# Kernel optimization log

Hardware: AMD Instinct MI355X
Metric: run time of the kernel (lower is better)

The kernel has to match this reference:

```python
import jax, jax.numpy as jnp
import numpy as np

BRANCH = 16   # children per internal node
DEPTH = 4     # levels 0..4, leaves at level 4
IN = 512
HID = 512

def _level_sizes():
    return [BRANCH ** d for d in range(DEPTH + 1)]

def setup_inputs() -> dict:
    key = jax.random.key(0)
    ks = jax.random.split(key, 9)
    N = sum(_level_sizes())  # 69905
    x = jax.random.normal(ks[0], (N, IN), dtype=jnp.float32)
    s = 1.0 / np.sqrt(IN + HID)  # torch nn.Linear default init bound
    def lin(kw, kb):
        w = jax.random.uniform(kw, (HID, IN + HID), jnp.float32, -s, s)
        b = jax.random.uniform(kb, (HID,), jnp.float32, -s, s)
        return w, b
    wi_w, wi_b = lin(ks[1], ks[2])
    wf_w, wf_b = lin(ks[3], ks[4])
    wo_w, wo_b = lin(ks[5], ks[6])
    wu_w, wu_b = lin(ks[7], ks[8])
    return {"x": x, "wi_w": wi_w, "wi_b": wi_b, "wf_w": wf_w, "wf_b": wf_b,
            "wo_w": wo_w, "wo_b": wo_b, "wu_w": wu_w, "wu_b": wu_b}

def reference(x, wi_w, wi_b, wf_w, wf_b, wo_w, wo_b, wu_w, wu_b):
    sizes = _level_sizes()
    offs = np.concatenate([[0], np.cumsum(sizes)])
    levels = [x[offs[d]:offs[d + 1]] for d in range(DEPTH + 1)]

    def gates(xh):
        i = jax.nn.sigmoid(xh @ wi_w.T + wi_b)
        o = jax.nn.sigmoid(xh @ wo_w.T + wo_b)
        u = jnp.tanh(xh @ wu_w.T + wu_b)
        return i, o, u

    # leaf_forward: h_prev = 0, no forget terms
    Xl = levels[DEPTH]
    xh = jnp.concatenate([Xl, jnp.zeros((Xl.shape[0], HID), Xl.dtype)], axis=1)
    i, o, u = gates(xh)
    C = i * u
    H = o * jnp.tanh(C)

    # node_forward, bottom-up. Faithful quirk of the source: the forget gate
    # is computed on the child CELL state (cat(x, c_k)), not the hidden state.
    for d in range(DEPTH - 1, -1, -1):
        Xd = levels[d]                      # [n, IN]
        n = Xd.shape[0]
        Hc = H.reshape(n, BRANCH, HID)      # children hidden
        Cc = C.reshape(n, BRANCH, HID)      # children cell
        h_sum = Hc.sum(axis=1)
        xh = jnp.concatenate([Xd, h_sum], axis=1)
        i, o, u = gates(xh)
        xc = jnp.concatenate([jnp.broadcast_to(Xd[:, None, :], (n, BRANCH, IN)), Cc], axis=-1)
        f = jax.nn.sigmoid(jnp.einsum('nbk,hk->nbh', xc, wf_w) + wf_b)
        C = i * u + (f * Cc).sum(axis=1)
        H = o * jnp.tanh(C)

    return H[0], C[0]
```

## Files before the change

### kernel.cpp

```cpp
#include <hip/hip_runtime.h>
#include <stdint.h>
#include <stddef.h>


typedef __bf16 bf16x8 __attribute__((ext_vector_type(8)));
typedef float  f32x4  __attribute__((ext_vector_type(4)));
typedef void __attribute__((address_space(3))) lds_void_t;
typedef void __attribute__((address_space(1))) gbl_void_t;

__device__ __forceinline__ uint16_t f2bf(float f) {
  union { __bf16 b; uint16_t u; } v;
  v.b = (__bf16)f;
  return v.u;
}
__device__ __forceinline__ float bf2f(uint16_t u) {
  union { uint32_t u; float f; } v; v.u = (uint32_t)u << 16;
  return v.f;
}
__device__ __forceinline__ float sig_(float x) {
  return __builtin_amdgcn_rcpf(1.0f + __expf(-x));
}
__device__ __forceinline__ float tanh_(float x) {
  return __builtin_fmaf(2.f,
      __builtin_amdgcn_rcpf(1.f + __expf(-2.f * x)), -1.f);
}

__global__ void k_conv_all(const float4* __restrict__ x,
                           ushort4* __restrict__ xdst, long n4x,
                           const float4* __restrict__ w0,
                           const float4* __restrict__ w1,
                           const float4* __restrict__ w2,
                           const float4* __restrict__ w3,
                           ushort4* __restrict__ wdst) {
  const long per4 = (long)512 * 1024 / 4;
  const long total = n4x + 4 * per4;
  long i = blockIdx.x * (long)blockDim.x + threadIdx.x;
  long stride = (long)gridDim.x * blockDim.x;
  for (; i < total; i += stride) {
    float4 v;
    ushort4* d;
    if (i < n4x) {
      v = x[i];
      d = xdst + i;
    } else {
      long j = i - n4x;
      long seg = j / per4, off2 = j - seg * per4;
      const float4* s = (seg == 0) ? w0 : (seg == 1) ? w1
                       : (seg == 2) ? w2 : w3;
      v = s[off2];
      d = wdst + j;
    }
    ushort4 r;
    r.x = f2bf(v.x); r.y = f2bf(v.y); r.z = f2bf(v.z); r.w = f2bf(v.w);
    *d = r;
  }
}

#define BM 128
#define BN 128
#define BK 32

__global__ __launch_bounds__(256, 3)
void k_leaf_fx(const uint16_t* __restrict__ Xleaf,
               const uint16_t* __restrict__ Wg,
               const float* __restrict__ bi, const float* __restrict__ bo,
               const float* __restrict__ bu,
               uint16_t* __restrict__ Cbf,
               const uint16_t* __restrict__ Xnext,
               uint16_t* __restrict__ xh_next,
               const uint16_t* __restrict__ Xbf,
               const uint16_t* __restrict__ Wf,
               float* __restrict__ FxAll) {
  __shared__ uint16_t smem[20480];
  const int tid = threadIdx.x, lane = tid & 63, wave = tid >> 6;
  const int lrow = lane & 15, quad = lane >> 4;

  if (blockIdx.x < 4096) {
    uint16_t* As = smem;
    uint16_t* Bs = smem + 8192;
    const int wm = (wave >> 1) * 64, wn = (wave & 1) * 32;
    long tm, tn;
    {
      const int nTm = 512;
      int b = blockIdx.x;
      int x = b & 7, j = b >> 3, per = nTm >> 3;
      tn = j & 7; tm = (long)x * per + (j >> 3);
    }
    f32x4 acc[3][4][2] = {};
    const int srow = lane >> 3;
    const int scol = (((lane & 7) ^ srow) << 3);
    const int rsw = lrow & 7;
    const int pc[2] = { ((0 + quad) ^ rsw) << 3, ((4 + quad) ^ rsw) << 3 };

    for (int k0 = 0; k0 < 512; k0 += 64) {
#pragma unroll
      for (int j = 0; j < 4; ++j) {
        int grp = wave * 4 + j;
        int row = grp * 8 + srow;
        const uint16_t* gp = Xleaf + (tm * 128 + row) * 512L + k0 + scol;
        __builtin_amdgcn_global_load_lds((gbl_void_t*)(uintptr_t)gp,
            (lds_void_t*)&As[grp * 512], 16, 0, 0);
      }
#pragma unroll
      for (int j = 0; j < 6; ++j) {
        int cc = wave * 6 + j;
        int g  = cc >> 3;
        long grow = (long)g * 512 + tn * 64 + (cc & 7) * 8 + srow;
        const uint16_t* gp = Wg + grow * 1024 + k0 + scol;
        __builtin_amdgcn_global_load_lds((gbl_void_t*)(uintptr_t)gp,
            (lds_void_t*)&Bs[cc * 512], 16, 0, 0);
      }
      __syncthreads();
#pragma unroll
      for (int h = 0; h < 2; ++h) {
        bf16x8 a[4];
#pragma unroll
        for (int f = 0; f < 4; ++f)
          a[f] = *(const bf16x8*)&As[(wm + f * 16 + lrow) * 64 + pc[h]];
#pragma unroll
        for (int g = 0; g < 3; ++g) {
          bf16x8 b0 = *(const bf16x8*)&Bs[(g * 64 + wn + lrow) * 64 + pc[h]];
          bf16x8 b1 = *(const bf16x8*)&Bs[(g * 64 + wn + 16 + lrow) * 64 +
                                          pc[h]];
#pragma unroll
          for (int fm = 0; fm < 4; ++fm) {
            acc[g][fm][0] = __builtin_amdgcn_mfma_f32_16x16x32_bf16(
                a[fm], b0, acc[g][fm][0], 0, 0, 0);
            acc[g][fm][1] = __builtin_amdgcn_mfma_f32_16x16x32_bf16(
                a[fm], b1, acc[g][fm][1], 0, 0, 0);
          }
        }
      }
      __syncthreads();
    }
#pragma unroll
    for (int fn = 0; fn < 2; ++fn) {
      long col = tn * 64 + wn + fn * 16 + lrow;
      float biv = bi[col], bov = bo[col], buv = bu[col];
#pragma unroll
      for (int fm = 0; fm < 4; ++fm) {
        long row0 = tm * 128 + wm + fm * 16 + quad * 4;
        long pg   = tm * 8 + (wm >> 4) + fm;
        float hs = 0.f;
#pragma unroll
        for (int r = 0; r < 4; ++r) {
          long row = row0 + r;
          float iv = sig_(acc[0][fm][fn][r] + biv);
          float ov = sig_(acc[1][fm][fn][r] + bov);
          float uv = tanh_(acc[2][fm][fn][r] + buv);
          float c  = iv * uv;
          Cbf[row * 512 + col] = f2bf(c);
          hs += ov * tanh_(c);
        }
        hs += __shfl_xor(hs, 16, 64);
        hs += __shfl_xor(hs, 32, 64);
        if (quad == 0) {
          xh_next[pg * 1024 + col]       = Xnext[pg * 512 + col];
          xh_next[pg * 1024 + 512 + col] = f2bf(hs);
        }
      }
    }
  } else {
    uint16_t* As = smem;
    uint16_t* Bs = smem + 4096;
    const int wm = (wave >> 1) * 64, wn = (wave & 1) * 64;
    int bid2 = (int)blockIdx.x - 4096;
    const long tm = bid2 % 35, tn = bid2 / 35;
    f32x4 acc[4][4] = {};
    const int srow2 = lane >> 2, scol2 = (lane & 3) * 8;
    for (int k0 = 0; k0 < 512; k0 += BK) {
#pragma unroll
      for (int i = 0; i < 2; ++i) {
        int row = i * 64 + wave * 16 + srow2;
        const uint16_t* gp = Xbf + (tm * BM + row) * 512L + k0 + scol2;
        __builtin_amdgcn_global_load_lds((gbl_void_t*)(uintptr_t)gp,
            (lds_void_t*)&As[i * 2048 + wave * 512], 16, 0, 0);
      }
#pragma unroll
      for (int i = 0; i < 2; ++i) {
        int row = i * 64 + wave * 16 + srow2;
        const uint16_t* gp = Wf + (tn * BN + row) * 1024L + k0 + scol2;
        __builtin_amdgcn_global_load_lds((gbl_void_t*)(uintptr_t)gp,
            (lds_void_t*)&Bs[i * 2048 + wave * 512], 16, 0, 0);
      }
      __syncthreads();
      bf16x8 a[4], b[4];
#pragma unroll
      for (int f = 0; f < 4; ++f)
        a[f] = *(const bf16x8*)&As[(wm + f * 16 + lrow) * BK + quad * 8];
#pragma unroll
      for (int f = 0; f < 4; ++f)
        b[f] = *(const bf16x8*)&Bs[(wn + f * 16 + lrow) * BK + quad * 8];
#pragma unroll
      for (int fm = 0; fm < 4; ++fm)
#pragma unroll
        for (int fn = 0; fn < 4; ++fn)
          acc[fm][fn] = __builtin_amdgcn_mfma_f32_16x16x32_bf16(
              a[fm], b[fn], acc[fm][fn], 0, 0, 0);
      __syncthreads();
    }
#pragma unroll
    for (int fm = 0; fm < 4; ++fm)
#pragma unroll
      for (int fn = 0; fn < 4; ++fn) {
        long col  = tn * BN + wn + fn * 16 + lrow;
        long row0 = tm * BM + wm + fm * 16 + quad * 4;
#pragma unroll
        for (int r = 0; r < 4; ++r)
          FxAll[(row0 + r) * 512 + col] = acc[fm][fn][r];
      }
  }
}

template <bool HAS_F, int MF>
__global__ __launch_bounds__(256, 3)
void k_level(const uint16_t* __restrict__ A, int lda, int K,
             const uint16_t* __restrict__ Wg,
             const float* __restrict__ bi, const float* __restrict__ bo,
             const float* __restrict__ bu,
             const float* __restrict__ Fpart,
             uint16_t* __restrict__ Cbf,
             const uint16_t* __restrict__ Xnext,
             uint16_t* __restrict__ xh_next) {
  constexpr int BMT = MF * 32;
  __shared__ uint16_t As[BMT * 64];
  __shared__ uint16_t Bs[192 * 64];
  const int tid = threadIdx.x, lane = tid & 63, wave = tid >> 6;
  const int lrow = lane & 15, quad = lane >> 4;
  const int wm = (wave >> 1) * (MF * 16), wn = (wave & 1) * 32;

  long tm, tn;
  {
    const int nTm = (int)(gridDim.x >> 3);
    int b = blockIdx.x;
    if ((nTm & 7) == 0) {
      int x = b & 7, j = b >> 3, per = nTm >> 3;
      tn = j & 7; tm = (long)x * per + (j >> 3);
    } else { tm = b >> 3; tn = b & 7; }
  }

  f32x4 acc[3][MF][2] = {};

  const int srow = lane >> 3;
  const int scol = (((lane & 7) ^ srow) << 3);
  const int rsw = lrow & 7;
  const int pc[2] = { ((0 + quad) ^ rsw) << 3, ((4 + quad) ^ rsw) << 3 };

  for (int k0 = 0; k0 < K; k0 += 64) {
#pragma unroll
    for (int j = 0; j < MF; ++j) {
      int grp = wave * MF + j;
      int row = grp * 8 + srow;
      const uint16_t* gp = A + (tm * BMT + row) * (long)lda + k0 + scol;
      __builtin_amdgcn_global_load_lds((gbl_void_t*)(uintptr_t)gp,
          (lds_void_t*)&As[grp * 512], 16, 0, 0);
    }
#pragma unroll
    for (int j = 0; j < 6; ++j) {
      int cc = wave * 6 + j;
      int g  = cc >> 3;
      long grow = (long)g * 512 + tn * 64 + (cc & 7) * 8 + srow;
      const uint16_t* gp = Wg + grow * 1024 + k0 + scol;
      __builtin_amdgcn_global_load_lds((gbl_void_t*)(uintptr_t)gp,
          (lds_void_t*)&Bs[cc * 512], 16, 0, 0);
    }
    __syncthreads();

#pragma unroll
    for (int h = 0; h < 2; ++h) {
      bf16x8 a[MF];
#pragma unroll
      for (int f = 0; f < MF; ++f)
        a[f] = *(const bf16x8*)&As[(wm + f * 16 + lrow) * 64 + pc[h]];
#pragma unroll
      for (int g = 0; g < 3; ++g) {
        bf16x8 b0 = *(const bf16x8*)&Bs[(g * 64 + wn + lrow) * 64 + pc[h]];
        bf16x8 b1 = *(const bf16x8*)&Bs[(g * 64 + wn + 16 + lrow) * 64 +
                                        pc[h]];
#pragma unroll
        for (int fm = 0; fm < MF; ++fm) {
          acc[g][fm][0] = __builtin_amdgcn_mfma_f32_16x16x32_bf16(
              a[fm], b0, acc[g][fm][0], 0, 0, 0);
          acc[g][fm][1] = __builtin_amdgcn_mfma_f32_16x16x32_bf16(
              a[fm], b1, acc[g][fm][1], 0, 0, 0);
        }
      }
    }
    __syncthreads();
  }

#pragma unroll
  for (int fn = 0; fn < 2; ++fn) {
    long col = tn * 64 + wn + fn * 16 + lrow;
    float biv = bi[col], bov = bo[col], buv = bu[col];
#pragma unroll
    for (int fm = 0; fm < MF; ++fm) {
      long row0 = tm * BMT + wm + fm * 16 + quad * 4;
      long pg   = tm * (BMT / 16) + (wm >> 4) + fm;
      float hs = 0.f;
#pragma unroll
      for (int r = 0; r < 4; ++r) {
        long row = row0 + r;
        float iv = sig_(acc[0][fm][fn][r] + biv);
        float ov = sig_(acc[1][fm][fn][r] + bov);
        float uv = tanh_(acc[2][fm][fn][r] + buv);
        float c  = iv * uv;
        if (HAS_F) c += Fpart[row * 512 + col];
        Cbf[row * 512 + col] = f2bf(c);
        hs += ov * tanh_(c);
      }
      hs += __shfl_xor(hs, 16, 64);
      hs += __shfl_xor(hs, 32, 64);
      if (quad == 0) {
        xh_next[pg * 1024 + col]       = Xnext[pg * 512 + col];
        xh_next[pg * 1024 + 512 + col] = f2bf(hs);
      }
    }
  }
}

template <int MF>
__global__ __launch_bounds__(256, 3)
void k_fc_combine(const uint16_t* __restrict__ Cbf,
                  const uint16_t* __restrict__ Wfc, int ldb,
                  const float* __restrict__ Fx,
                  const float* __restrict__ bfb,
                  float* __restrict__ Fpart) {
  constexpr int BMT = MF * 32;
  __shared__ uint16_t As[BMT * 64];
  __shared__ uint16_t Bs[128 * 64];
  const int tid = threadIdx.x, lane = tid & 63, wave = tid >> 6;
  const int lrow = lane & 15, quad = lane >> 4;
  const int wm = (wave >> 1) * (MF * 16), wn = (wave & 1) * 64;
  long tm, tn;
  {
    const int nTm = (int)(gridDim.x >> 2);
    int b = blockIdx.x;
    if ((nTm & 7) == 0) {
      int x = b & 7, j = b >> 3, per = nTm >> 3;
      tn = j & 3; tm = (long)x * per + (j >> 2);
    } else { tm = b >> 2; tn = b & 3; }
  }
  const int lda = 512;
  f32x4 acc[MF][4] = {};

  const int srow = lane >> 3;
  const int scol = (((lane & 7) ^ srow) << 3);
  const int rsw = lrow & 7;
  const int pc[2] = { ((0 + quad) ^ rsw) << 3, ((4 + quad) ^ rsw) << 3 };

  for (int k0 = 0; k0 < 512; k0 += 64) {
#pragma unroll
    for (int j = 0; j < MF; ++j) {
      int grp = wave * MF + j;
      int row = grp * 8 + srow;
      const uint16_t* gp = Cbf + (tm * BMT + row) * (long)lda + k0 + scol;
      __builtin_amdgcn_global_load_lds((gbl_void_t*)(uintptr_t)gp,
          (lds_void_t*)&As[grp * 512], 16, 0, 0);
    }
#pragma unroll
    for (int j = 0; j < 4; ++j) {
      int row = wave * 32 + j * 8 + srow;
      const uint16_t* gp = Wfc + (tn * BN + row) * (long)ldb + k0 + scol;
      __builtin_amdgcn_global_load_lds((gbl_void_t*)(uintptr_t)gp,
          (lds_void_t*)&Bs[(wave * 32 + j * 8) * 64], 16, 0, 0);
    }
    __syncthreads();
#pragma unroll
    for (int h = 0; h < 2; ++h) {
      bf16x8 a[MF], b[4];
#pragma unroll
      for (int f = 0; f < MF; ++f)
        a[f] = *(const bf16x8*)&As[(wm + f * 16 + lrow) * 64 + pc[h]];
#pragma unroll
      for (int f = 0; f < 4; ++f)
        b[f] = *(const bf16x8*)&Bs[(wn + f * 16 + lrow) * 64 + pc[h]];
#pragma unroll
      for (int fm = 0; fm < MF; ++fm)
#pragma unroll
        for (int fn = 0; fn < 4; ++fn)
          acc[fm][fn] = __builtin_amdgcn_mfma_f32_16x16x32_bf16(
              a[fm], b[fn], acc[fm][fn], 0, 0, 0);
    }
    __syncthreads();
  }
#pragma unroll
  for (int fm = 0; fm < MF; ++fm) {
    long pg   = tm * (BMT / 16) + (wm >> 4) + fm;
    long row0 = tm * BMT + wm + fm * 16 + quad * 4;
#pragma unroll
    for (int fn = 0; fn < 4; ++fn) {
      long col = tn * BN + wn + fn * 16 + lrow;
      float fx = Fx[pg * 512 + col] + bfb[col];
      float t = 0.f;
#pragma unroll
      for (int r = 0; r < 4; ++r)
        t += sig_(fx + acc[fm][fn][r]) * bf2f(Cbf[(row0 + r) * 512 + col]);
      t += __shfl_xor(t, 16, 64);
      t += __shfl_xor(t, 32, 64);
      if (quad == 0) Fpart[pg * 512 + col] = t;
    }
  }
}

__global__ __launch_bounds__(256)
void k_fcdot(const uint16_t* __restrict__ Cbf,
             const uint16_t* __restrict__ Wfc,
             const float* __restrict__ Fx,
             const float* __restrict__ bfb,
             float* __restrict__ Fpart,
             const uint16_t* __restrict__ xhC,
             const uint16_t* __restrict__ Wg,
             float* __restrict__ Gf) {
  __shared__ uint16_t smem[12288];
  const int tid = threadIdx.x, lane = tid & 63, wave = tid >> 6;
  if (blockIdx.x < 16) {
    uint16_t* As = smem;
    uint16_t* Bs = smem + 4096;
    const int lrow = lane & 15, quad = lane >> 4;
    const int wm = (wave >> 1) * 32, wn = (wave & 1) * 64;
    int b = blockIdx.x;
    long tm = b >> 2, tn = b & 3;
    f32x4 acc[2][4] = {};
    const int srow = lane >> 3;
    const int scol = (((lane & 7) ^ srow) << 3);
    const int rsw = lrow & 7;
    const int pc[2] = { ((0 + quad) ^ rsw) << 3, ((4 + quad) ^ rsw) << 3 };
    for (int k0 = 0; k0 < 512; k0 += 64) {
#pragma unroll
      for (int j = 0; j < 2; ++j) {
        int grp = wave * 2 + j;
        int row = grp * 8 + srow;
        const uint16_t* gp = Cbf + (tm * 64 + row) * 512L + k0 + scol;
        __builtin_amdgcn_global_load_lds((gbl_void_t*)(uintptr_t)gp,
            (lds_void_t*)&As[grp * 512], 16, 0, 0);
      }
#pragma unroll
      for (int j = 0; j < 4; ++j) {
        int row = wave * 32 + j * 8 + srow;
        const uint16_t* gp = Wfc + (tn * 128 + row) * 1024L + k0 + scol;
        __builtin_amdgcn_global_load_lds((gbl_void_t*)(uintptr_t)gp,
            (lds_void_t*)&Bs[(wave * 32 + j * 8) * 64], 16, 0, 0);
      }
      __syncthreads();
#pragma unroll
      for (int h = 0; h < 2; ++h) {
        bf16x8 a[2], bb[4];
#pragma unroll
        for (int f = 0; f < 2; ++f)
          a[f] = *(const bf16x8*)&As[(wm + f * 16 + lrow) * 64 + pc[h]];
#pragma unroll
        for (int f = 0; f < 4; ++f)
          bb[f] = *(const bf16x8*)&Bs[(wn + f * 16 + lrow) * 64 + pc[h]];
#pragma unroll
        for (int fm = 0; fm < 2; ++fm)
#pragma unroll
          for (int fn = 0; fn < 4; ++fn)
            acc[fm][fn] = __builtin_amdgcn_mfma_f32_16x16x32_bf16(
                a[fm], bb[fn], acc[fm][fn], 0, 0, 0);
      }
      __syncthreads();
    }
#pragma unroll
    for (int fm = 0; fm < 2; ++fm) {
      long pg   = tm * 4 + (wm >> 4) + fm;
      long row0 = tm * 64 + wm + fm * 16 + quad * 4;
#pragma unroll
      for (int fn = 0; fn < 4; ++fn) {
        long col = tn * 128 + wn + fn * 16 + lrow;
        float fx = Fx[pg * 512 + col] + bfb[col];
        float t = 0.f;
#pragma unroll
        for (int r = 0; r < 4; ++r)
          t += sig_(fx + acc[fm][fn][r]) * bf2f(Cbf[(row0 + r) * 512 + col]);
        t += __shfl_xor(t, 16, 64);
        t += __shfl_xor(t, 32, 64);
        if (quad == 0) Fpart[pg * 512 + col] = t;
      }
    }
  } else {
    int wid = (int)(((long)(blockIdx.x - 16) * 256 + tid) >> 6);
    if (wid >= 16 * 1536) return;
    int m = wid / 1536, n = wid - m * 1536;
    const uint16_t* a = xhC + (long)m * 1024;
    const uint16_t* b = Wg + (long)n * 1024;
    int k0 = lane * 16;
    float s = 0.f;
#pragma unroll
    for (int j = 0; j < 16; j += 4) {
      ushort4 av = *(const ushort4*)(a + k0 + j);
      ushort4 bv = *(const ushort4*)(b + k0 + j);
      s += bf2f(av.x) * bf2f(bv.x) + bf2f(av.y) * bf2f(bv.y)
         + bf2f(av.z) * bf2f(bv.z) + bf2f(av.w) * bf2f(bv.w);
    }
#pragma unroll
    for (int off = 32; off; off >>= 1) s += __shfl_xor(s, off, 64);
    if (lane == 0) Gf[(long)m * 1536 + n] = s;
  }
}

__global__ void k_dot_merge(const uint16_t* __restrict__ xhC,
                            const uint16_t* __restrict__ Wg,
                            float* __restrict__ Gf,
                            const float* __restrict__ CupA,
                            const float* __restrict__ WfF,
                            float* __restrict__ Fc) {
  int wid  = (int)((blockIdx.x * (long)blockDim.x + threadIdx.x) >> 6);
  int lane = threadIdx.x & 63;
  if (wid < 1536) {
    const uint16_t* a = xhC;
    const uint16_t* b = Wg + (long)wid * 1024;
    int k0 = lane * 16;
    float s = 0.f;
#pragma unroll
    for (int j = 0; j < 16; j += 4) {
      ushort4 av = *(const ushort4*)(a + k0 + j);
      ushort4 bv = *(const ushort4*)(b + k0 + j);
      s += bf2f(av.x) * bf2f(bv.x) + bf2f(av.y) * bf2f(bv.y)
         + bf2f(av.z) * bf2f(bv.z) + bf2f(av.w) * bf2f(bv.w);
    }
#pragma unroll
    for (int off = 32; off; off >>= 1) s += __shfl_xor(s, off, 64);
    if (lane == 0) Gf[wid] = s;
  } else {
    int w2 = wid - 1536;
    if (w2 >= 16 * 512) return;
    int m = w2 >> 9, n = w2 & 511;
    const float* a = CupA + (long)m * 512;
    const float* b = WfF + (long)n * 1024;
    int k0 = lane * 8;
    float s = 0.f;
#pragma unroll
    for (int j = 0; j < 8; j += 4) {
      float4 av = *(const float4*)(a + k0 + j);
      float4 bv = *(const float4*)(b + k0 + j);
      s += av.x * bv.x + av.y * bv.y + av.z * bv.z + av.w * bv.w;
    }
#pragma unroll
    for (int off = 32; off; off >>= 1) s += __shfl_xor(s, off, 64);
    if (lane == 0) Fc[(long)m * 512 + n] = s;
  }
}

__global__ __launch_bounds__(1024)
void k_lvl1_tail(const float* __restrict__ G,
                 const float* __restrict__ Fpart,
                 const float* __restrict__ bi,
                 const float* __restrict__ bo,
                 const float* __restrict__ bu,
                 float* __restrict__ Cv,
                 const uint16_t* __restrict__ xroot,
                 uint16_t* __restrict__ xh) {
  __shared__ float Hl[16 * 512];
  const int tid = threadIdx.x;
#pragma unroll
  for (int it = 0; it < 2; ++it) {
    int idx = it * 1024 + tid;
    int p = idx >> 7, hq = (idx & 127) << 2;
    const float* g = G + (long)p * 1536;
    float4 gi = *(const float4*)(g + hq);
    float4 go = *(const float4*)(g + 512 + hq);
    float4 gu = *(const float4*)(g + 1024 + hq);
    float4 b_i = *(const float4*)(bi + hq);
    float4 b_o = *(const float4*)(bo + hq);
    float4 b_u = *(const float4*)(bu + hq);
    float4 fp = *(const float4*)(Fpart + (long)p * 512 + hq);
    const float* gip = &gi.x; const float* gop = &go.x;
    const float* gup = &gu.x; const float* bip = &b_i.x;
    const float* bop = &b_o.x; const float* bup = &b_u.x;
    const float* fpp = &fp.x;
    float4 hv, cv;
    float* hvp = &hv.x; float* cvp = &cv.x;
#pragma unroll
    for (int j = 0; j < 4; ++j) {
      float iv = sig_(gip[j] + bip[j]);
      float ov = sig_(gop[j] + bop[j]);
      float uv = tanh_(gup[j] + bup[j]);
      float c  = iv * uv + fpp[j];
      cvp[j] = c;
      hvp[j] = ov * tanh_(c);
    }
    *(float4*)(Cv + (long)p * 512 + hq) = cv;
    *(float4*)(&Hl[p * 512 + hq]) = hv;
  }
  __syncthreads();
  if (tid < 128) {
    int hq = tid << 2;
    float4 s = {0.f, 0.f, 0.f, 0.f};
#pragma unroll
    for (int b = 0; b < 16; ++b) {
      float4 v = *(const float4*)(&Hl[b * 512 + hq]);
      s.x += v.x; s.y += v.y; s.z += v.z; s.w += v.w;
    }
    *(ushort4*)(xh + hq) = *(const ushort4*)(xroot + hq);
    ushort4 hw = {f2bf(s.x), f2bf(s.y), f2bf(s.z), f2bf(s.w)};
    *(ushort4*)(xh + 512 + hq) = hw;
  }
}

__global__ void k_root_tail(const float* __restrict__ Fc,
                            const float* __restrict__ Fx,
                            const float* __restrict__ bfb,
                            const float* __restrict__ Cc,
                            const float* __restrict__ G,
                            const float* __restrict__ bi,
                            const float* __restrict__ bo,
                            const float* __restrict__ bu,
                            float* __restrict__ H, float* __restrict__ Cv) {
  int hq = (threadIdx.x & 127) << 2;
  float4 fxv = *(const float4*)(Fx + hq);
  float4 bfv = *(const float4*)(bfb + hq);
  float fx0 = fxv.x + bfv.x, fx1 = fxv.y + bfv.y;
  float fx2 = fxv.z + bfv.z, fx3 = fxv.w + bfv.w;
  float a0 = 0.f, a1 = 0.f, a2 = 0.f, a3 = 0.f;
#pragma unroll 4
  for (int b = 0; b < 16; ++b) {
    float4 f = *(const float4*)(Fc + (long)b * 512 + hq);
    float4 c = *(const float4*)(Cc + (long)b * 512 + hq);
    a0 += sig_(fx0 + f.x) * c.x;
    a1 += sig_(fx1 + f.y) * c.y;
    a2 += sig_(fx2 + f.z) * c.z;
    a3 += sig_(fx3 + f.w) * c.w;
  }
  float fpp[4] = {a0, a1, a2, a3};
  float4 gi = *(const float4*)(G + hq);
  float4 go = *(const float4*)(G + 512 + hq);
  float4 gu = *(const float4*)(G + 1024 + hq);
  float4 b_i = *(const float4*)(bi + hq);
  float4 b_o = *(const float4*)(bo + hq);
  float4 b_u = *(const float4*)(bu + hq);
  const float* gip = &gi.x; const float* gop = &go.x; const float* gup = &gu.x;
  const float* bip = &b_i.x; const float* bop = &b_o.x; const float* bup = &b_u.x;
  float4 hv, cv;
  float* hvp = &hv.x; float* cvp = &cv.x;
#pragma unroll
  for (int j = 0; j < 4; ++j) {
    float iv = sig_(gip[j] + bip[j]);
    float ov = sig_(gop[j] + bop[j]);
    float uv = tanh_(gup[j] + bup[j]);
    float c  = iv * uv + fpp[j];
    cvp[j] = c;
    hvp[j] = ov * tanh_(c);
  }
  *(float4*)(H  + hq) = hv;
  *(float4*)(Cv + hq) = cv;
}

extern "C" void kernel_launch(void* const* d_in, const int* in_sizes, int n_in,
                              void* d_out, int out_size, void* d_ws, size_t ws_size,
                              hipStream_t stream) {
  const float* x    = (const float*)d_in[0];
  const float* wi_w = (const float*)d_in[1];
  const float* wi_b = (const float*)d_in[2];
  const float* wf_w = (const float*)d_in[3];
  const float* wf_b = (const float*)d_in[4];
  const float* wo_w = (const float*)d_in[5];
  const float* wo_b = (const float*)d_in[6];
  const float* wu_w = (const float*)d_in[7];
  const float* wu_b = (const float*)d_in[8];
  (void)in_sizes; (void)n_in; (void)out_size; (void)ws_size;

  static const long offs[5] = {0, 1, 17, 273, 4369};
  const long NTOT = 69905;

  char* ws = (char*)d_ws;
  size_t off = 0;
  auto alloc = [&](size_t bytes) -> void* {
    void* p = ws + off;
    off += (bytes + 255) & ~(size_t)255;
    return p;
  };
  uint16_t* Xbf   = (uint16_t*)alloc(NTOT * 512 * 2);
  uint16_t* Wgw   = (uint16_t*)alloc((size_t)2048 * 1024 * 2);
  uint16_t* Wg    = Wgw;
  uint16_t* Wf    = Wgw + (size_t)1536 * 1024;
  float*    FxAll = (float*)alloc((size_t)4480 * 512 * 4);
  uint16_t* Cbf   = (uint16_t*)alloc((size_t)65536 * 512 * 2);
  uint16_t* CbfU  = (uint16_t*)alloc((size_t)4096 * 512 * 2);
  uint16_t* CbfU2 = (uint16_t*)alloc((size_t)256 * 512 * 2);
  uint16_t* xhA   = (uint16_t*)alloc((size_t)4096 * 1024 * 2);
  uint16_t* xhB   = (uint16_t*)alloc((size_t)256 * 1024 * 2);
  uint16_t* xhC   = (uint16_t*)alloc((size_t)16 * 1024 * 2);
  float*    Fpart = (float*)alloc((size_t)4096 * 512 * 4);
  float*    Gf    = (float*)alloc((size_t)16 * 1536 * 4);
  float*    Fc    = (float*)alloc((size_t)16 * 512 * 4);
  float*    CupA  = (float*)alloc((size_t)16 * 512 * 4);

  {
    long n4x = NTOT * 512 / 4;
    k_conv_all<<<8192, 256, 0, stream>>>(
        (const float4*)x, (ushort4*)Xbf, n4x,
        (const float4*)wi_w, (const float4*)wo_w,
        (const float4*)wu_w, (const float4*)wf_w, (ushort4*)Wgw);
  }

  k_leaf_fx<<<4236, 256, 0, stream>>>(
      Xbf + offs[4] * 512, Wg, wi_b, wo_b, wu_b,
      Cbf, Xbf + offs[3] * 512, xhA,
      Xbf, Wf, FxAll);
  k_fc_combine<4><<<2048, 256, 0, stream>>>(Cbf, Wf + 512, 1024,
                                            FxAll + offs[3] * 512, wf_b, Fpart);

  k_level<true, 2><<<512, 256, 0, stream>>>(
      xhA, 1024, 1024, Wg, wi_b, wo_b, wu_b, Fpart,
      CbfU, Xbf + offs[2] * 512, xhB);
  k_fc_combine<2><<<256, 256, 0, stream>>>(CbfU, Wf + 512, 1024,
                                           FxAll + offs[2] * 512, wf_b, Fpart);

  k_level<true, 2><<<32, 256, 0, stream>>>(
      xhB, 1024, 1024, Wg, wi_b, wo_b, wu_b, Fpart,
      CbfU2, Xbf + offs[1] * 512, xhC);

  k_fcdot<<<6160, 256, 0, stream>>>(CbfU2, Wf + 512,
                                    FxAll + offs[1] * 512, wf_b, Fpart,
                                    xhC, Wg, Gf);

  k_lvl1_tail<<<1, 1024, 0, stream>>>(Gf, Fpart, wi_b, wo_b, wu_b,
                                      CupA, Xbf + offs[0] * 512, xhC);

  {
    long waves = 1536 + 16L * 512;
    k_dot_merge<<<(int)(waves / 4), 256, 0, stream>>>(
        xhC, Wg, Gf, CupA, wf_w + 512, Fc);
  }
  k_root_tail<<<1, 128, 0, stream>>>(Fc, FxAll, wf_b, CupA, Gf,
                                     wi_b, wo_b, wu_b,
                                     (float*)d_out, (float*)d_out + 512);
}
```

Baseline: 471.8 us.

## Co-schedule forget-gate GEMM with next-level gate GEMM and split gate epilogue

The level-3 and level-2 gate GEMMs (on xh) do not depend on the child forget-gate sums. Each is now launched in the same grid as the preceding forget-gate combine kernel, with raw gate pre-activations written to a new fp32 G3 buffer. A small elementwise kernel then adds Fpart, applies the nonlinearities and builds the next xh. This cuts serial launches and fills idle CUs in the small level kernels, at the cost of an extra fp32 round-trip through global memory for the gate outputs.

```diff
diff --git a/kernel.cpp b/kernel.cpp
--- a/kernel.cpp
+++ b/kernel.cpp
@@ -81,9 +81,8 @@
     const int wm = (wave >> 1) * 64, wn = (wave & 1) * 32;
     long tm, tn;
     {
-      const int nTm = 512;
       int b = blockIdx.x;
-      int x = b & 7, j = b >> 3, per = nTm >> 3;
+      int x = b & 7, j = b >> 3, per = 64;
       tn = j & 7; tm = (long)x * per + (j >> 3);
     }
     f32x4 acc[3][4][2] = {};
@@ -212,193 +211,340 @@
   }
 }
 
-template <bool HAS_F, int MF>
 __global__ __launch_bounds__(256, 3)
-void k_level(const uint16_t* __restrict__ A, int lda, int K,
-             const uint16_t* __restrict__ Wg,
-             const float* __restrict__ bi, const float* __restrict__ bo,
-             const float* __restrict__ bu,
-             const float* __restrict__ Fpart,
-             uint16_t* __restrict__ Cbf,
-             const uint16_t* __restrict__ Xnext,
-             uint16_t* __restrict__ xh_next) {
-  constexpr int BMT = MF * 32;
-  __shared__ uint16_t As[BMT * 64];
-  __shared__ uint16_t Bs[192 * 64];
+void k_fc4_l3g(const uint16_t* __restrict__ Cbf,
+               const uint16_t* __restrict__ Wfc,
+               const float* __restrict__ Fx,
+               const float* __restrict__ bfb,
+               float* __restrict__ Fpart,
+               const uint16_t* __restrict__ xhA,
+               const uint16_t* __restrict__ Wg,
+               float* __restrict__ G3) {
+  __shared__ uint16_t smem[16384];
   const int tid = threadIdx.x, lane = tid & 63, wave = tid >> 6;
   const int lrow = lane & 15, quad = lane >> 4;
-  const int wm = (wave >> 1) * (MF * 16), wn = (wave & 1) * 32;
-
-  long tm, tn;
-  {
-    const int nTm = (int)(gridDim.x >> 3);
-    int b = blockIdx.x;
-    if ((nTm & 7) == 0) {
-      int x = b & 7, j = b >> 3, per = nTm >> 3;
-      tn = j & 7; tm = (long)x * per + (j >> 3);
-    } else { tm = b >> 3; tn = b & 7; }
-  }
-
-  f32x4 acc[3][MF][2] = {};
-
   const int srow = lane >> 3;
   const int scol = (((lane & 7) ^ srow) << 3);
   const int rsw = lrow & 7;
   const int pc[2] = { ((0 + quad) ^ rsw) << 3, ((4 + quad) ^ rsw) << 3 };
 
-  for (int k0 = 0; k0 < K; k0 += 64) {
-#pragma unroll
-    for (int j = 0; j < MF; ++j) {
-      int grp = wave * MF + j;
-      int row = grp * 8 + srow;
-      const uint16_t* gp = A + (tm * BMT + row) * (long)lda + k0 + scol;
-      __builtin_amdgcn_global_load_lds((gbl_void_t*)(uintptr_t)gp,
-          (lds_void_t*)&As[grp * 512], 16, 0, 0);
-    }
-#pragma unroll
-    for (int j = 0; j < 6; ++j) {
-      int cc = wave * 6 + j;
-      int g  = cc >> 3;
-      long grow = (long)g * 512 + tn * 64 + (cc & 7) * 8 + srow;
-      const uint16_t* gp = Wg + grow * 1024 + k0 + scol;
-      __builtin_amdgcn_global_load_lds((gbl_void_t*)(uintptr_t)gp,
-          (lds_void_t*)&Bs[cc * 512], 16, 0, 0);
-    }
-    __syncthreads();
-
-#pragma unroll
-    for (int h = 0; h < 2; ++h) {
-      bf16x8 a[MF];
-#pragma unroll
-      for (int f = 0; f < MF; ++f)
-        a[f] = *(const bf16x8*)&As[(wm + f * 16 + lrow) * 64 + pc[h]];
-#pragma unroll
-      for (int g = 0; g < 3; ++g) {
-        bf16x8 b0 = *(const bf16x8*)&Bs[(g * 64 + wn + lrow) * 64 + pc[h]];
-        bf16x8 b1 = *(const bf16x8*)&Bs[(g * 64 + wn + 16 + lrow) * 64 +
-                                        pc[h]];
-#pragma unroll
-        for (int fm = 0; fm < MF; ++fm) {
-          acc[g][fm][0] = __builtin_amdgcn_mfma_f32_16x16x32_bf16(
-              a[fm], b0, acc[g][fm][0], 0, 0, 0);
-          acc[g][fm][1] = __builtin_amdgcn_mfma_f32_16x16x32_bf16(
-              a[fm], b1, acc[g][fm][1], 0, 0, 0);
+  if (blockIdx.x < 2048) {
+    uint16_t* As = smem;
+    uint16_t* Bs = smem + 8192;
+    const int wm = (wave >> 1) * 64, wn = (wave & 1) * 64;
+    long tm, tn;
+    {
+      int b = blockIdx.x;
+      int x = b & 7, j = b >> 3, per = 64;
+      tn = j & 3; tm = (long)x * per + (j >> 2);
+    }
+    f32x4 acc[4][4] = {};
+    for (int k0 = 0; k0 < 512; k0 += 64) {
+#pragma unroll
+      for (int j = 0; j < 4; ++j) {
+        int grp = wave * 4 + j;
+        int row = grp * 8 + srow;
+        const uint16_t* gp = Cbf + (tm * 128 + row) * 512L + k0 + scol;
+        __builtin_amdgcn_global_load_lds((gbl_void_t*)(uintptr_t)gp,
+            (lds_void_t*)&As[grp * 512], 16, 0, 0);
+      }
+#pragma unroll
+      for (int j = 0; j < 4; ++j) {
+        int row = wave * 32 + j * 8 + srow;
+        const uint16_t* gp = Wfc + (tn * BN + row) * 1024L + k0 + scol;
+        __builtin_amdgcn_global_load_lds((gbl_void_t*)(uintptr_t)gp,
+            (lds_void_t*)&Bs[(wave * 32 + j * 8) * 64], 16, 0, 0);
+      }
+      __syncthreads();
+#pragma unroll
+      for (int h = 0; h < 2; ++h) {
+        bf16x8 a[4], b[4];
+#pragma unroll
+        for (int f = 0; f < 4; ++f)
+          a[f] = *(const bf16x8*)&As[(wm + f * 16 + lrow) * 64 + pc[h]];
+#pragma unroll
+        for (int f = 0; f < 4; ++f)
+          b[f] = *(const bf16x8*)&Bs[(wn + f * 16 + lrow) * 64 + pc[h]];
+#pragma unroll
+        for (int fm = 0; fm < 4; ++fm)
+#pragma unroll
+          for (int fn = 0; fn < 4; ++fn)
+            acc[fm][fn] = __builtin_amdgcn_mfma_f32_16x16x32_bf16(
+                a[fm], b[fn], acc[fm][fn], 0, 0, 0);
+      }
+      __syncthreads();
+    }
+#pragma unroll
+    for (int fm = 0; fm < 4; ++fm) {
+      long pg   = tm * 8 + (wm >> 4) + fm;
+      long row0 = tm * 128 + wm + fm * 16 + quad * 4;
+#pragma unroll
+      for (int fn = 0; fn < 4; ++fn) {
+        long col = tn * BN + wn + fn * 16 + lrow;
+        float fx = Fx[pg * 512 + col] + bfb[col];
+        float t = 0.f;
+#pragma unroll
+        for (int r = 0; r < 4; ++r)
+          t += sig_(fx + acc[fm][fn][r]) * bf2f(Cbf[(row0 + r) * 512 + col]);
+        t += __shfl_xor(t, 16, 64);
+        t += __shfl_xor(t, 32, 64);
+        if (quad == 0) Fpart[pg * 512 + col] = t;
+      }
+    }
+  } else {
+    uint16_t* As = smem;
+    uint16_t* Bs = smem + 4096;
+    const int wm = (wave >> 1) * 32, wn = (wave & 1) * 32;
+    long tm, tn;
+    {
+      int b = (int)blockIdx.x - 2048;
+      int x = b & 7, j = b >> 3, per = 8;
+      tn = j & 7; tm = (long)x * per + (j >> 3);
+    }
+    f32x4 acc[3][2][2] = {};
+    for (int k0 = 0; k0 < 1024; k0 += 64) {
+#pragma unroll
+      for (int j = 0; j < 2; ++j) {
+        int grp = wave * 2 + j;
+        int row = grp * 8 + srow;
+        const uint16_t* gp = xhA + (tm * 64 + row) * 1024L + k0 + scol;
+        __builtin_amdgcn_global_load_lds((gbl_void_t*)(uintptr_t)gp,
+            (lds_void_t*)&As[grp * 512], 16, 0, 0);
+      }
+#pragma unroll
+      for (int j = 0; j < 6; ++j) {
+        int cc = wave * 6 + j;
+        int g  = cc >> 3;
+        long grow = (long)g * 512 + tn * 64 + (cc & 7) * 8 + srow;
+        const uint16_t* gp = Wg + grow * 1024 + k0 + scol;
+        __builtin_amdgcn_global_load_lds((gbl_void_t*)(uintptr_t)gp,
+            (lds_void_t*)&Bs[cc * 512], 16, 0, 0);
+      }
+      __syncthreads();
+#pragma unroll
+      for (int h = 0; h < 2; ++h) {
+        bf16x8 a[2];
+#pragma unroll
+        for (int f = 0; f < 2; ++f)
+          a[f] = *(const bf16x8*)&As[(wm + f * 16 + lrow) * 64 + pc[h]];
+#pragma unroll
+        for (int g = 0; g < 3; ++g) {
+          bf16x8 b0 = *(const bf16x8*)&Bs[(g * 64 + wn + lrow) * 64 + pc[h]];
+          bf16x8 b1 = *(const bf16x8*)&Bs[(g * 64 + wn + 16 + lrow) * 64 +
+                                          pc[h]];
+#pragma unroll
+          for (int fm = 0; fm < 2; ++fm) {
+            acc[g][fm][0] = __builtin_amdgcn_mfma_f32_16x16x32_bf16(
+                a[fm], b0, acc[g][fm][0], 0, 0, 0);
+            acc[g][fm][1] = __builtin_amdgcn_mfma_f32_16x16x32_bf16(
+                a[fm], b1, acc[g][fm][1], 0, 0, 0);
+          }
         }
       }
-    }
-    __syncthreads();
-  }
-
-#pragma unroll
-  for (int fn = 0; fn < 2; ++fn) {
-    long col = tn * 64 + wn + fn * 16 + lrow;
-    float biv = bi[col], bov = bo[col], buv = bu[col];
-#pragma unroll
-    for (int fm = 0; fm < MF; ++fm) {
-      long row0 = tm * BMT + wm + fm * 16 + quad * 4;
-      long pg   = tm * (BMT / 16) + (wm >> 4) + fm;
-      float hs = 0.f;
-#pragma unroll
-      for (int r = 0; r < 4; ++r) {
-        long row = row0 + r;
-        float iv = sig_(acc[0][fm][fn][r] + biv);
-        float ov = sig_(acc[1][fm][fn][r] + bov);
-        float uv = tanh_(acc[2][fm][fn][r] + buv);
-        float c  = iv * uv;
-        if (HAS_F) c += Fpart[row * 512 + col];
-        Cbf[row * 512 + col] = f2bf(c);
-        hs += ov * tanh_(c);
-      }
-      hs += __shfl_xor(hs, 16, 64);
-      hs += __shfl_xor(hs, 32, 64);
-      if (quad == 0) {
-        xh_next[pg * 1024 + col]       = Xnext[pg * 512 + col];
-        xh_next[pg * 1024 + 512 + col] = f2bf(hs);
-      }
-    }
-  }
-}
-
-template <int MF>
+      __syncthreads();
+    }
+#pragma unroll
+    for (int fn = 0; fn < 2; ++fn) {
+      long col = tn * 64 + wn + fn * 16 + lrow;
+#pragma unroll
+      for (int fm = 0; fm < 2; ++fm) {
+        long row0 = tm * 64 + wm + fm * 16 + quad * 4;
+#pragma unroll
+        for (int r = 0; r < 4; ++r) {
+          long row = row0 + r;
+#pragma unroll
+          for (int g = 0; g < 3; ++g)
+            G3[row * 1536 + g * 512 + col] = acc[g][fm][fn][r];
+        }
+      }
+    }
+  }
+}
+
+__global__ void k_level_final(const float* __restrict__ G3,
+                              const float* __restrict__ Fpart,
+                              const float* __restrict__ bi,
+                              const float* __restrict__ bo,
+                              const float* __restrict__ bu,
+                              uint16_t* __restrict__ Cbf_out,
+                              const uint16_t* __restrict__ Xnext,
+                              uint16_t* __restrict__ xh_next) {
+  const long p = blockIdx.x;
+  const int hq = (threadIdx.x & 127) << 2;
+  float4 b_i = *(const float4*)(bi + hq);
+  float4 b_o = *(const float4*)(bo + hq);
+  float4 b_u = *(const float4*)(bu + hq);
+  const float* bip = &b_i.x; const float* bop = &b_o.x;
+  const float* bup = &b_u.x;
+  float hs[4] = {0.f, 0.f, 0.f, 0.f};
+#pragma unroll 4
+  for (int k = 0; k < 16; ++k) {
+    long row = p * 16 + k;
+    float4 gi = *(const float4*)(G3 + row * 1536 + hq);
+    float4 go = *(const float4*)(G3 + row * 1536 + 512 + hq);
+    float4 gu = *(const float4*)(G3 + row * 1536 + 1024 + hq);
+    float4 fp = *(const float4*)(Fpart + row * 512 + hq);
+    const float* gip = &gi.x; const float* gop = &go.x;
+    const float* gup = &gu.x; const float* fpp = &fp.x;
+    ushort4 cw; unsigned short* cwp = &cw.x;
+#pragma unroll
+    for (int j = 0; j < 4; ++j) {
+      float iv = sig_(gip[j] + bip[j]);
+      float ov = sig_(gop[j] + bop[j]);
+      float uv = tanh_(gup[j] + bup[j]);
+      float c  = iv * uv + fpp[j];
+      cwp[j] = f2bf(c);
+      hs[j] += ov * tanh_(c);
+    }
+    *(ushort4*)(Cbf_out + row * 512 + hq) = cw;
+  }
+  *(ushort4*)(xh_next + p * 1024 + hq) = *(const ushort4*)(Xnext + p * 512 + hq);
+  ushort4 hw = {f2bf(hs[0]), f2bf(hs[1]), f2bf(hs[2]), f2bf(hs[3])};
+  *(ushort4*)(xh_next + p * 1024 + 512 + hq) = hw;
+}
+
 __global__ __launch_bounds__(256, 3)
-void k_fc_combine(const uint16_t* __restrict__ Cbf,
-                  const uint16_t* __restrict__ Wfc, int ldb,
-                  const float* __restrict__ Fx,
-                  const float* __restrict__ bfb,
-                  float* __restrict__ Fpart) {
-  constexpr int BMT = MF * 32;
-  __shared__ uint16_t As[BMT * 64];
-  __shared__ uint16_t Bs[128 * 64];
+void k_fc2_l2g(const uint16_t* __restrict__ CbfU,
+               const uint16_t* __restrict__ Wfc,
+               const float* __restrict__ Fx,
+               const float* __restrict__ bfb,
+               float* __restrict__ Fpart,
+               const uint16_t* __restrict__ xhB,
+               const uint16_t* __restrict__ Wg,
+               float* __restrict__ G3) {
+  __shared__ uint16_t smem[16384];
   const int tid = threadIdx.x, lane = tid & 63, wave = tid >> 6;
   const int lrow = lane & 15, quad = lane >> 4;
-  const int wm = (wave >> 1) * (MF * 16), wn = (wave & 1) * 64;
-  long tm, tn;
-  {
-    const int nTm = (int)(gridDim.x >> 2);
-    int b = blockIdx.x;
-    if ((nTm & 7) == 0) {
-      int x = b & 7, j = b >> 3, per = nTm >> 3;
-      tn = j & 3; tm = (long)x * per + (j >> 2);
-    } else { tm = b >> 2; tn = b & 3; }
-  }
-  const int lda = 512;
-  f32x4 acc[MF][4] = {};
-
   const int srow = lane >> 3;
   const int scol = (((lane & 7) ^ srow) << 3);
   const int rsw = lrow & 7;
   const int pc[2] = { ((0 + quad) ^ rsw) << 3, ((4 + quad) ^ rsw) << 3 };
 
-  for (int k0 = 0; k0 < 512; k0 += 64) {
-#pragma unroll
-    for (int j = 0; j < MF; ++j) {
-      int grp = wave * MF + j;
-      int row = grp * 8 + srow;
-      const uint16_t* gp = Cbf + (tm * BMT + row) * (long)lda + k0 + scol;
-      __builtin_amdgcn_global_load_lds((gbl_void_t*)(uintptr_t)gp,
-          (lds_void_t*)&As[grp * 512], 16, 0, 0);
-    }
-#pragma unroll
-    for (int j = 0; j < 4; ++j) {
-      int row = wave * 32 + j * 8 + srow;
-      const uint16_t* gp = Wfc + (tn * BN + row) * (long)ldb + k0 + scol;
-      __builtin_amdgcn_global_load_lds((gbl_void_t*)(uintptr_t)gp,
-          (lds_void_t*)&Bs[(wave * 32 + j * 8) * 64], 16, 0, 0);
-    }
-    __syncthreads();
-#pragma unroll
-    for (int h = 0; h < 2; ++h) {
-      bf16x8 a[MF], b[4];
-#pragma unroll
-      for (int f = 0; f < MF; ++f)
-        a[f] = *(const bf16x8*)&As[(wm + f * 16 + lrow) * 64 + pc[h]];
-#pragma unroll
-      for (int f = 0; f < 4; ++f)
-        b[f] = *(const bf16x8*)&Bs[(wn + f * 16 + lrow) * 64 + pc[h]];
-#pragma unroll
-      for (int fm = 0; fm < MF; ++fm)
-#pragma unroll
-        for (int fn = 0; fn < 4; ++fn)
-          acc[fm][fn] = __builtin_amdgcn_mfma_f32_16x16x32_bf16(
-              a[fm], b[fn], acc[fm][fn], 0, 0, 0);
-    }
-    __syncthreads();
-  }
-#pragma unroll
-  for (int fm = 0; fm < MF; ++fm) {
-    long pg   = tm * (BMT / 16) + (wm >> 4) + fm;
-    long row0 = tm * BMT + wm + fm * 16 + quad * 4;
-#pragma unroll
-    for (int fn = 0; fn < 4; ++fn) {
-      long col = tn * BN + wn + fn * 16 + lrow;
-      float fx = Fx[pg * 512 + col] + bfb[col];
-      float t = 0.f;
-#pragma unroll
-      for (int r = 0; r < 4; ++r)
-        t += sig_(fx + acc[fm][fn][r]) * bf2f(Cbf[(row0 + r) * 512 + col]);
-      t += __shfl_xor(t, 16, 64);
-      t += __shfl_xor(t, 32, 64);
-      if (quad == 0) Fpart[pg * 512 + col] = t;
+  if (blockIdx.x < 256) {
+    uint16_t* As = smem;
+    uint16_t* Bs = smem + 4096;
+    const int wm = (wave >> 1) * 32, wn = (wave & 1) * 64;
+    long tm, tn;
+    {
+      int b = blockIdx.x;
+      int x = b & 7, j = b >> 3, per = 8;
+      tn = j & 3; tm = (long)x * per + (j >> 2);
+    }
+    f32x4 acc[2][4] = {};
+    for (int k0 = 0; k0 < 512; k0 += 64) {
+#pragma unroll
+      for (int j = 0; j < 2; ++j) {
+        int grp = wave * 2 + j;
+        int row = grp * 8 + srow;
+        const uint16_t* gp = CbfU + (tm * 64 + row) * 512L + k0 + scol;
+        __builtin_amdgcn_global_load_lds((gbl_void_t*)(uintptr_t)gp,
+            (lds_void_t*)&As[grp * 512], 16, 0, 0);
+      }
+#pragma unroll
+      for (int j = 0; j < 4; ++j) {
+        int row = wave * 32 + j * 8 + srow;
+        const uint16_t* gp = Wfc + (tn * BN + row) * 1024L + k0 + scol;
+        __builtin_amdgcn_global_load_lds((gbl_void_t*)(uintptr_t)gp,
+            (lds_void_t*)&Bs[(wave * 32 + j * 8) * 64], 16, 0, 0);
+      }
+      __syncthreads();
+#pragma unroll
+      for (int h = 0; h < 2; ++h) {
+        bf16x8 a[2], b[4];
+#pragma unroll
+        for (int f = 0; f < 2; ++f)
+          a[f] = *(const bf16x8*)&As[(wm + f * 16 + lrow) * 64 + pc[h]];
+#pragma unroll
+        for (int f = 0; f < 4; ++f)
+          b[f] = *(const bf16x8*)&Bs[(wn + f * 16 + lrow) * 64 + pc[h]];
+#pragma unroll
+        for (int fm = 0; fm < 2; ++fm)
+#pragma unroll
+          for (int fn = 0; fn < 4; ++fn)
+            acc[fm][fn] = __builtin_amdgcn_mfma_f32_16x16x32_bf16(
+                a[fm], b[fn], acc[fm][fn], 0, 0, 0);
+      }
+      __syncthreads();
+    }
+#pragma unroll
+    for (int fm = 0; fm < 2; ++fm) {
+      long pg   = tm * 4 + (wm >> 4) + fm;
+      long row0 = tm * 64 + wm + fm * 16 + quad * 4;
+#pragma unroll
+      for (int fn = 0; fn < 4; ++fn) {
+        long col = tn * BN + wn + fn * 16 + lrow;
+        float fx = Fx[pg * 512 + col] + bfb[col];
+        float t = 0.f;
+#pragma unroll
+        for (int r = 0; r < 4; ++r)
+          t += sig_(fx + acc[fm][fn][r]) * bf2f(CbfU[(row0 + r) * 512 + col]);
+        t += __shfl_xor(t, 16, 64);
+        t += __shfl_xor(t, 32, 64);
+        if (quad == 0) Fpart[pg * 512 + col] = t;
+      }
+    }
+  } else {
+    uint16_t* As = smem;
+    uint16_t* Bs = smem + 4096;
+    const int wm = (wave >> 1) * 32, wn = (wave & 1) * 32;
+    int b = (int)blockIdx.x - 256;
+    long tm = b >> 3, tn = b & 7;
+    f32x4 acc[3][2][2] = {};
+    for (int k0 = 0; k0 < 1024; k0 += 64) {
+#pragma unroll
+      for (int j = 0; j < 2; ++j) {
+        int grp = wave * 2 + j;
+        int row = grp * 8 + srow;
+        const uint16_t* gp = xhB + (tm * 64 + row) * 1024L + k0 + scol;
+        __builtin_amdgcn_global_load_lds((gbl_void_t*)(uintptr_t)gp,
+            (lds_void_t*)&As[grp * 512], 16, 0, 0);
+      }
+#pragma unroll
+      for (int j = 0; j < 6; ++j) {
+        int cc = wave * 6 + j;
+        int g  = cc >> 3;
+        long grow = (long)g * 512 + tn * 64 + (cc & 7) * 8 + srow;
+        const uint16_t* gp = Wg + grow * 1024 + k0 + scol;
+        __builtin_amdgcn_global_load_lds((gbl_void_t*)(uintptr_t)gp,
+            (lds_void_t*)&Bs[cc * 512], 16, 0, 0);
+      }
+      __syncthreads();
+#pragma unroll
+      for (int h = 0; h < 2; ++h) {
+        bf16x8 a[2];
+#pragma unroll
+        for (int f = 0; f < 2; ++f)
+          a[f] = *(const bf16x8*)&As[(wm + f * 16 + lrow) * 64 + pc[h]];
+#pragma unroll
+        for (int g = 0; g < 3; ++g) {
+          bf16x8 b0 = *(const bf16x8*)&Bs[(g * 64 + wn + lrow) * 64 + pc[h]];
+          bf16x8 b1 = *(const bf16x8*)&Bs[(g * 64 + wn + 16 + lrow) * 64 +
+                                          pc[h]];
+#pragma unroll
+          for (int fm = 0; fm < 2; ++fm) {
+            acc[g][fm][0] = __builtin_amdgcn_mfma_f32_16x16x32_bf16(
+                a[fm], b0, acc[g][fm][0], 0, 0, 0);
+            acc[g][fm][1] = __builtin_amdgcn_mfma_f32_16x16x32_bf16(
+                a[fm], b1, acc[g][fm][1], 0, 0, 0);
+          }
+        }
+      }
+      __syncthreads();
+    }
+#pragma unroll
+    for (int fn = 0; fn < 2; ++fn) {
+      long col = tn * 64 + wn + fn * 16 + lrow;
+#pragma unroll
+      for (int fm = 0; fm < 2; ++fm) {
+        long row0 = tm * 64 + wm + fm * 16 + quad * 4;
+#pragma unroll
+        for (int r = 0; r < 4; ++r) {
+          long row = row0 + r;
+#pragma unroll
+          for (int g = 0; g < 3; ++g)
+            G3[row * 1536 + g * 512 + col] = acc[g][fm][fn][r];
+        }
+      }
     }
   }
 }
@@ -682,6 +828,7 @@
   uint16_t* xhB   = (uint16_t*)alloc((size_t)256 * 1024 * 2);
   uint16_t* xhC   = (uint16_t*)alloc((size_t)16 * 1024 * 2);
   float*    Fpart = (float*)alloc((size_t)4096 * 512 * 4);
+  float*    G3    = (float*)alloc((size_t)4096 * 1536 * 4);
   float*    Gf    = (float*)alloc((size_t)16 * 1536 * 4);
   float*    Fc    = (float*)alloc((size_t)16 * 512 * 4);
   float*    CupA  = (float*)alloc((size_t)16 * 512 * 4);
@@ -698,18 +845,20 @@
       Xbf + offs[4] * 512, Wg, wi_b, wo_b, wu_b,
       Cbf, Xbf + offs[3] * 512, xhA,
       Xbf, Wf, FxAll);
-  k_fc_combine<4><<<2048, 256, 0, stream>>>(Cbf, Wf + 512, 1024,
-                                            FxAll + offs[3] * 512, wf_b, Fpart);
-
-  k_level<true, 2><<<512, 256, 0, stream>>>(
-      xhA, 1024, 1024, Wg, wi_b, wo_b, wu_b, Fpart,
-      CbfU, Xbf + offs[2] * 512, xhB);
-  k_fc_combine<2><<<256, 256, 0, stream>>>(CbfU, Wf + 512, 1024,
-                                           FxAll + offs[2] * 512, wf_b, Fpart);
-
-  k_level<true, 2><<<32, 256, 0, stream>>>(
-      xhB, 1024, 1024, Wg, wi_b, wo_b, wu_b, Fpart,
-      CbfU2, Xbf + offs[1] * 512, xhC);
+
+  k_fc4_l3g<<<2560, 256, 0, stream>>>(
+      Cbf, Wf + 512, FxAll + offs[3] * 512, wf_b, Fpart,
+      xhA, Wg, G3);
+
+  k_level_final<<<256, 128, 0, stream>>>(
+      G3, Fpart, wi_b, wo_b, wu_b, CbfU, Xbf + offs[2] * 512, xhB);
+
+  k_fc2_l2g<<<288, 256, 0, stream>>>(
+      CbfU, Wf + 512, FxAll + offs[2] * 512, wf_b, Fpart,
+      xhB, Wg, G3);
+
+  k_level_final<<<16, 128, 0, stream>>>(
+      G3, Fpart, wi_b, wo_b, wu_b, CbfU2, Xbf + offs[1] * 512, xhC);
 
   k_fcdot<<<6160, 256, 0, stream>>>(CbfU2, Wf + 512,
                                     FxAll + offs[1] * 512, wf_b, Fpart,
```

New measurement: 473.1 us (median of 2 runs). No clear change (+0.3%).
